# Kernel tuning notes

Measured on AMD Instinct MI355X. Metric: run time of the kernel, lower is better.

The kernel has to match this reference:

```python
import jax, jax.numpy as jnp
from jax import lax
import numpy as np

K = 3          # sampling grid size (kernel_size)
WS = 4         # scope kernel size (weight_shape)
DILATION = 1


def setup_inputs() -> dict:
    key = jax.random.key(0)
    k1, k2, k3, k4 = jax.random.split(key, 4)
    x = jax.random.normal(k1, (4, 128, 56, 56), jnp.float32)
    # offset conv is zero-initialized in the original; use small values so offsets are realistic
    offset_w = jax.random.normal(k2, (2 * K * K, 128, K, K), jnp.float32) * 0.01
    offset_b = jax.random.normal(k3, (2 * K * K,), jnp.float32) * 0.01
    weight = jax.random.normal(k4, (128, WS, WS), jnp.float32) * 0.1  # depthwise scope kernel
    return {"x": x, "offset_w": offset_w, "offset_b": offset_b, "weight": weight}


def reference(x, offset_w, offset_b, weight):
    B, C, H, W = x.shape
    K2 = K * K
    # offset conv: 3x3, stride 1, pad 1 (same geometry as main conv)
    off = lax.conv_general_dilated(
        x, offset_w, window_strides=(1, 1), padding=[(1, 1), (1, 1)],
        dimension_numbers=("NCHW", "OIHW", "NCHW"))
    off = off + offset_b[None, :, None, None]
    off = off * DILATION                     # offset_clip is None
    off = off.reshape(B, K2, 2, H, W)
    dy, dx = off[:, :, 0], off[:, :, 1]      # [B,K2,H,W]

    # base coordinates of the KxK sampling grid centered inside the WSxWS scope kernel
    base = jnp.arange(K, dtype=x.dtype) - (K - 1) / 2 + (WS - 1) / 2   # [K]
    by = jnp.repeat(base, K)                 # k = i*K + j -> row i
    bx = jnp.tile(base, K)                   # k = i*K + j -> col j
    yc = dy + by[None, :, None, None]        # [B,K2,H,W] sampling coords in kernel space
    xc = dx + bx[None, :, None, None]

    # bilinear sampling of the scope kernel (zero outside scope)
    wflat = weight.reshape(C, WS * WS)
    y0 = jnp.floor(yc)
    x0 = jnp.floor(xc)
    samp = jnp.zeros((C, B, K2, H, W), x.dtype)
    for oy, ox in ((0, 0), (0, 1), (1, 0), (1, 1)):
        yi = y0 + oy
        xi = x0 + ox
        coef = (1.0 - jnp.abs(yc - yi)) * (1.0 - jnp.abs(xc - xi))
        valid = (yi >= 0) & (yi < WS) & (xi >= 0) & (xi < WS)
        idx = (jnp.clip(yi, 0, WS - 1) * WS + jnp.clip(xi, 0, WS - 1)).astype(jnp.int32)
        vals = jnp.take(wflat, idx, axis=1)  # [C,B,K2,H,W] irregular gather
        samp = samp + (coef * valid)[None] * vals
    samp = jnp.moveaxis(samp, 0, 1)          # [B,C,K2,H,W]

    # depthwise conv with per-pixel sampled kernels (stride 1, pad 1, dilation 1)
    xp = jnp.pad(x, ((0, 0), (0, 0), (1, 1), (1, 1)))
    pats = jnp.stack([xp[:, :, i:i + H, j:j + W] for i in range(K) for j in range(K)], axis=2)
    return jnp.sum(samp * pats, axis=2)      # [B,C,H,W]
```

## Files before the change

### kernel.cpp

```cpp
#include <hip/hip_runtime.h>

#define CC 128
#define HH 56
#define WW 56
#define NK2 9
#define NO 18
#define WSZ 4
#define W64 64
#define NCG 16
#define SCG 8
#define CPG 16

#define WSA_FLOATS (224L * NCG * NO * W64)
#define WSC_ENTRIES (4L * NK2 * HH * W64)

__global__ __launch_bounds__(256, 4) void conv_partial(
    const float* __restrict__ x,
    const float* __restrict__ offset_w,
    float* __restrict__ wsA)
{
    const int blk = blockIdx.x;
    const int cg  = blk & 15;
    const int bh4 = blk >> 4;
    const int b   = bh4 / 14;
    const int h4  = bh4 - b * 14;
    const int h0  = h4 * 4;
    const int t   = threadIdx.x;
    const int lane = t & 63;
    const int wv  = __builtin_amdgcn_readfirstlane(t >> 6);

    __shared__ float s_red[4][2][NO][W64];

    float acc[4][NO];
    #pragma unroll
    for (int r = 0; r < 4; ++r)
        #pragma unroll
        for (int o = 0; o < NO; ++o) acc[r][o] = 0.f;

    if (lane < WW) {
        #pragma unroll
        for (int ci = 0; ci < 2; ++ci) {
            const int c = cg * 8 + wv * 2 + ci;
            const float* xc = x + ((long)b * CC + c) * HH * WW;
            float xr[6][3];
            #pragma unroll
            for (int r6 = 0; r6 < 6; ++r6) {
                const int hy = h0 + r6 - 1;
                float v0 = 0.f, v1 = 0.f, v2 = 0.f;
                if (hy >= 0 && hy < HH) {
                    const float* row = xc + hy * WW;
                    v1 = row[lane];
                    v0 = (lane > 0)      ? row[lane - 1] : 0.f;
                    v2 = (lane < WW - 1) ? row[lane + 1] : 0.f;
                }
                xr[r6][0] = v0; xr[r6][1] = v1; xr[r6][2] = v2;
            }
            const float* wc = offset_w + c * 9;
            #pragma unroll
            for (int o = 0; o < NO; ++o) {
                const float* wo = wc + o * (CC * 9);
                float w9[9];
                #pragma unroll
                for (int j = 0; j < 9; ++j) w9[j] = wo[j];
                #pragma unroll
                for (int ky = 0; ky < 3; ++ky)
                    #pragma unroll
                    for (int kx = 0; kx < 3; ++kx) {
                        const float wf = w9[ky * 3 + kx];
                        #pragma unroll
                        for (int r = 0; r < 4; ++r)
                            acc[r][o] += wf * xr[r + ky][kx];
                    }
            }
        }
    }

    const float* sr = (const float*)s_red;
    #pragma unroll
    for (int round = 0; round < 2; ++round) {
        #pragma unroll
        for (int r2 = 0; r2 < 2; ++r2)
            #pragma unroll
            for (int o = 0; o < NO; ++o)
                s_red[wv][r2][o][lane] = acc[round * 2 + r2][o];
        __syncthreads();
        for (int s = t; s < 2 * NO * W64; s += 256) {
            const float v = sr[s] + sr[2304 + s] + sr[2 * 2304 + s] + sr[3 * 2304 + s];
            const int r2  = s / (NO * W64);
            const int rem = s - r2 * (NO * W64);
            const int bh  = b * HH + h0 + round * 2 + r2;
            wsA[((long)bh * NCG + cg) * (NO * W64) + rem] = v;
        }
        __syncthreads();
    }
}

__global__ __launch_bounds__(64) void coef_kernel(
    const float* __restrict__ wsA,
    const float* __restrict__ offset_b,
    float4* __restrict__ wsC,
    unsigned* __restrict__ wsI)
{
    const int blk = blockIdx.x;
    const int k2  = blk % NK2;
    const int bh  = blk / NK2;
    const int b   = bh / HH;
    const int h   = bh - b * HH;
    const int w   = threadIdx.x;

    const float* base = wsA + (long)bh * (NCG * NO * W64);
    float dy = offset_b[2 * k2];
    float dx = offset_b[2 * k2 + 1];
    #pragma unroll
    for (int g = 0; g < NCG; ++g) {
        dy += base[g * (NO * W64) + (2 * k2) * W64 + w];
        dx += base[g * (NO * W64) + (2 * k2 + 1) * W64 + w];
    }

    const float yc = dy + 0.5f + (float)(k2 / 3);
    const float xc = dx + 0.5f + (float)(k2 % 3);
    const float y0 = floorf(yc), x0f = floorf(xc);
    const float fy = yc - y0, fx = xc - x0f;
    const int yi = (int)y0, xi = (int)x0f;
    float cf[4]; int id[4];
    #pragma unroll
    for (int q = 0; q < 4; ++q) {
        const int oy = q >> 1, ox = q & 1;
        const int yy = yi + oy, xx = xi + ox;
        float c2 = (oy ? fy : 1.f - fy) * (ox ? fx : 1.f - fx);
        const bool valid = (yy >= 0) && (yy < WSZ) && (xx >= 0) && (xx < WSZ);
        cf[q] = valid ? c2 : 0.f;
        const int yyc = yy < 0 ? 0 : (yy > 3 ? 3 : yy);
        const int xxc = xx < 0 ? 0 : (xx > 3 ? 3 : xx);
        id[q] = yyc * 4 + xxc;
    }
    const long oidx = ((long)(b * NK2 + k2) * HH + h) * W64 + w;
    wsC[oidx] = make_float4(cf[0], cf[1], cf[2], cf[3]);
    wsI[oidx] = (unsigned)(id[0] | (id[1] << 4) | (id[2] << 8) | (id[3] << 12));
}

__global__ __launch_bounds__(256) void sample_kernel(
    const float* __restrict__ x,
    const float* __restrict__ weight,
    const float4* __restrict__ wsC,
    const unsigned* __restrict__ wsI,
    float* __restrict__ out)
{
    const int blk = blockIdx.x;
    const int bh  = blk >> 3;
    const int cg  = blk & 7;
    const int b   = bh / HH;
    const int h   = bh - b * HH;
    const int t   = threadIdx.x;
    const int lane = t & 63;
    const int wv  = __builtin_amdgcn_readfirstlane(t >> 6);

    __shared__ float s_wT[16][20];
    if (t < 256) {
        const int j = t >> 4, cl = t & 15;
        s_wT[j][cl] = weight[(cg * CPG + cl) * 16 + j];
    }
    __syncthreads();

    if (lane >= WW) return;
    const int w = lane;
    const int cl0 = wv * 4;

    float4 cf[NK2]; unsigned pk[NK2];
    const long cidx0 = ((long)b * NK2 * HH + h) * W64 + w;
    #pragma unroll
    for (int k2 = 0; k2 < NK2; ++k2) {
        cf[k2] = wsC[cidx0 + (long)k2 * HH * W64];
        pk[k2] = wsI[cidx0 + (long)k2 * HH * W64];
    }

    float xv[4][9];
    #pragma unroll
    for (int u = 0; u < 4; ++u) {
        const int c = cg * CPG + cl0 + u;
        const float* xc = x + ((long)b * CC + c) * HH * WW;
        #pragma unroll
        for (int ky = 0; ky < 3; ++ky) {
            const int hy = h + ky - 1;
            #pragma unroll
            for (int kx = 0; kx < 3; ++kx) {
                const int wx = w + kx - 1;
                float v = 0.f;
                if (hy >= 0 && hy < HH && wx >= 0 && wx < WW)
                    v = xc[hy * WW + wx];
                xv[u][ky * 3 + kx] = v;
            }
        }
    }

    float res[4] = {0.f, 0.f, 0.f, 0.f};
    #pragma unroll
    for (int k2 = 0; k2 < NK2; ++k2) {
        const unsigned p = pk[k2];
        const float4 W0 = *(const float4*)&s_wT[p & 15][cl0];
        const float4 W1 = *(const float4*)&s_wT[(p >> 4) & 15][cl0];
        const float4 W2 = *(const float4*)&s_wT[(p >> 8) & 15][cl0];
        const float4 W3 = *(const float4*)&s_wT[(p >> 12) & 15][cl0];
        const float4 c4 = cf[k2];
        res[0] += (c4.x * W0.x + c4.y * W1.x + c4.z * W2.x + c4.w * W3.x) * xv[0][k2];
        res[1] += (c4.x * W0.y + c4.y * W1.y + c4.z * W2.y + c4.w * W3.y) * xv[1][k2];
        res[2] += (c4.x * W0.z + c4.y * W1.z + c4.z * W2.z + c4.w * W3.z) * xv[2][k2];
        res[3] += (c4.x * W0.w + c4.y * W1.w + c4.z * W2.w + c4.w * W3.w) * xv[3][k2];
    }

    #pragma unroll
    for (int u = 0; u < 4; ++u) {
        const int c = cg * CPG + cl0 + u;
        out[(((long)b * CC + c) * HH + h) * WW + w] = res[u];
    }
}

extern "C" void kernel_launch(void* const* d_in, const int* in_sizes, int n_in,
                              void* d_out, int out_size, void* d_ws, size_t ws_size,
                              hipStream_t stream) {
    const float* x        = (const float*)d_in[0];
    const float* offset_w = (const float*)d_in[1];
    const float* offset_b = (const float*)d_in[2];
    const float* weight   = (const float*)d_in[3];
    float* out = (float*)d_out;

    char* p = (char*)d_ws;
    float*    wsA = (float*)p;                          p += WSA_FLOATS * 4;
    float4*   wsC = (float4*)p;                         p += WSC_ENTRIES * 16;
    unsigned* wsI = (unsigned*)p;

    conv_partial <<<4 * 14 * NCG, 256, 0, stream>>>(x, offset_w, wsA);
    coef_kernel  <<<224 * NK2, 64, 0, stream>>>(wsA, offset_b, wsC, wsI);
    sample_kernel<<<224 * SCG, 256, 0, stream>>>(x, weight, wsC, wsI, out);
}
```

Before: 95.41 us.

## Stage input rows in LDS and split offset channels across twice the waves

The offset-conv partial kernel now runs 512 threads per block and splits the 18 output offset channels into two halves of 9, with each pair of waves sharing the same 2 input channels. Input rows, including halo and zero padding, are loaded once into shared memory instead of through per-lane global loads with boundary branches. This halves the per-thread accumulator count, which lowers register pressure and doubles the wave parallelism on this stage. In exchange it adds an extra barrier and shared-memory staging, and the larger blocks may limit occupancy.

```diff
diff --git a/kernel.cpp b/kernel.cpp
--- a/kernel.cpp
+++ b/kernel.cpp
@@ -14,7 +14,7 @@
 #define WSA_FLOATS (224L * NCG * NO * W64)
 #define WSC_ENTRIES (4L * NK2 * HH * W64)
 
-__global__ __launch_bounds__(256, 4) void conv_partial(
+__global__ __launch_bounds__(512, 4) void conv_partial(
     const float* __restrict__ x,
     const float* __restrict__ offset_w,
     float* __restrict__ wsA)
@@ -29,49 +29,62 @@
     const int lane = t & 63;
     const int wv  = __builtin_amdgcn_readfirstlane(t >> 6);
 
+    __shared__ float s_x[8][6][68];
     __shared__ float s_red[4][2][NO][W64];
 
-    float acc[4][NO];
+    const int c0 = cg * 8;
+
+    for (int i = t; i < 8 * 6 * 68; i += 512) {
+        const int cl  = i / 408;
+        const int rem = i - cl * 408;
+        const int r6  = rem / 68;
+        const int col = rem - r6 * 68;
+        const int wx  = col - 1;
+        const int hy  = h0 + r6 - 1;
+        float v = 0.f;
+        if (wx >= 0 && wx < WW && hy >= 0 && hy < HH)
+            v = x[(((long)b * CC + c0 + cl) * HH + hy) * WW + wx];
+        s_x[cl][r6][col] = v;
+    }
+    __syncthreads();
+
+    const int pair = wv >> 1;
+    const int half = wv & 1;
+
+    float acc[4][9];
     #pragma unroll
     for (int r = 0; r < 4; ++r)
         #pragma unroll
-        for (int o = 0; o < NO; ++o) acc[r][o] = 0.f;
-
-    if (lane < WW) {
-        #pragma unroll
-        for (int ci = 0; ci < 2; ++ci) {
-            const int c = cg * 8 + wv * 2 + ci;
-            const float* xc = x + ((long)b * CC + c) * HH * WW;
-            float xr[6][3];
-            #pragma unroll
-            for (int r6 = 0; r6 < 6; ++r6) {
-                const int hy = h0 + r6 - 1;
-                float v0 = 0.f, v1 = 0.f, v2 = 0.f;
-                if (hy >= 0 && hy < HH) {
-                    const float* row = xc + hy * WW;
-                    v1 = row[lane];
-                    v0 = (lane > 0)      ? row[lane - 1] : 0.f;
-                    v2 = (lane < WW - 1) ? row[lane + 1] : 0.f;
+        for (int oo = 0; oo < 9; ++oo) acc[r][oo] = 0.f;
+
+    #pragma unroll
+    for (int cl2 = 0; cl2 < 2; ++cl2) {
+        const int cl = pair * 2 + cl2;
+        const int c  = c0 + cl;
+
+        float xr[6][3];
+        #pragma unroll
+        for (int r6 = 0; r6 < 6; ++r6)
+            #pragma unroll
+            for (int k = 0; k < 3; ++k)
+                xr[r6][k] = s_x[cl][r6][lane + k];
+
+        const float* wc = offset_w + ((long)half * 9 * CC + c) * 9;
+        #pragma unroll
+        for (int oo = 0; oo < 9; ++oo) {
+            const float* wo = wc + oo * (CC * 9);
+            float w9[9];
+            #pragma unroll
+            for (int j = 0; j < 9; ++j) w9[j] = wo[j];
+            #pragma unroll
+            for (int ky = 0; ky < 3; ++ky)
+                #pragma unroll
+                for (int kx = 0; kx < 3; ++kx) {
+                    const float wf = w9[ky * 3 + kx];
+                    #pragma unroll
+                    for (int r = 0; r < 4; ++r)
+                        acc[r][oo] += wf * xr[r + ky][kx];
                 }
-                xr[r6][0] = v0; xr[r6][1] = v1; xr[r6][2] = v2;
-            }
-            const float* wc = offset_w + c * 9;
-            #pragma unroll
-            for (int o = 0; o < NO; ++o) {
-                const float* wo = wc + o * (CC * 9);
-                float w9[9];
-                #pragma unroll
-                for (int j = 0; j < 9; ++j) w9[j] = wo[j];
-                #pragma unroll
-                for (int ky = 0; ky < 3; ++ky)
-                    #pragma unroll
-                    for (int kx = 0; kx < 3; ++kx) {
-                        const float wf = w9[ky * 3 + kx];
-                        #pragma unroll
-                        for (int r = 0; r < 4; ++r)
-                            acc[r][o] += wf * xr[r + ky][kx];
-                    }
-            }
         }
     }
 
@@ -81,10 +94,10 @@
         #pragma unroll
         for (int r2 = 0; r2 < 2; ++r2)
             #pragma unroll
-            for (int o = 0; o < NO; ++o)
-                s_red[wv][r2][o][lane] = acc[round * 2 + r2][o];
+            for (int oo = 0; oo < 9; ++oo)
+                s_red[pair][r2][half * 9 + oo][lane] = acc[round * 2 + r2][oo];
         __syncthreads();
-        for (int s = t; s < 2 * NO * W64; s += 256) {
+        for (int s = t; s < 2 * NO * W64; s += 512) {
             const float v = sr[s] + sr[2304 + s] + sr[2 * 2304 + s] + sr[3 * 2304 + s];
             const int r2  = s / (NO * W64);
             const int rem = s - r2 * (NO * W64);
@@ -229,7 +242,7 @@
     float4*   wsC = (float4*)p;                         p += WSC_ENTRIES * 16;
     unsigned* wsI = (unsigned*)p;
 
-    conv_partial <<<4 * 14 * NCG, 256, 0, stream>>>(x, offset_w, wsA);
+    conv_partial <<<4 * 14 * NCG, 512, 0, stream>>>(x, offset_w, wsA);
     coef_kernel  <<<224 * NK2, 64, 0, stream>>>(wsA, offset_b, wsC, wsI);
     sample_kernel<<<224 * SCG, 256, 0, stream>>>(x, weight, wsC, wsI, out);
 }
```

Result: slower. 99.91 us (+4.7%).

## Compute offset conv with bf16 MFMA and fuse coefficient computation

Applied to the files above, without the earlier changes.

Replaces the scalar FP32 offset convolution and its separate partial-sum reduction and coefficient kernels with one kernel per output row. That kernel stages x in LDS as bf16 and runs the 3x3 conv as an implicit GEMM on 16x16x32 bf16 MFMA instructions. Bilinear coefficients are then computed directly from the LDS results. A small prep kernel repacks offset_w into MFMA A-fragment layout each call. This removes the global workspace round-trip and one launch, but lowers offset precision to bf16, which can shift floor() boundaries in the sampling coordinates.

```diff
diff --git a/kernel.cpp b/kernel.cpp
--- a/kernel.cpp
+++ b/kernel.cpp
@@ -7,136 +7,123 @@
 #define NO 18
 #define WSZ 4
 #define W64 64
-#define NCG 16
 #define SCG 8
 #define CPG 16
 
-#define WSA_FLOATS (224L * NCG * NO * W64)
+typedef __attribute__((ext_vector_type(8))) short short8;
+typedef __attribute__((ext_vector_type(4))) float f32x4;
+
+#define WSW_SHORTS  (9L * 2 * 4 * 64 * 8)
 #define WSC_ENTRIES (4L * NK2 * HH * W64)
 
-__global__ __launch_bounds__(256, 4) void conv_partial(
+__device__ __forceinline__ unsigned short f2bf(float f) {
+    unsigned u = __builtin_bit_cast(unsigned, f);
+    u = u + 0x7fffu + ((u >> 16) & 1u);
+    return (unsigned short)(u >> 16);
+}
+
+__global__ __launch_bounds__(256) void prep_afrag(
+    const float* __restrict__ offset_w,
+    unsigned short* __restrict__ wsW)
+{
+    const int e = blockIdx.x * 256 + threadIdx.x;
+    if (e >= (int)WSW_SHORTS) return;
+    const int j    = e & 7;
+    const int lane = (e >> 3) & 63;
+    const int kt   = (e >> 9) & 3;
+    const int mt   = (e >> 11) & 1;
+    const int k9   = e >> 12;
+    const int o = mt * 16 + (lane & 15);
+    const int c = kt * 32 + (lane >> 4) * 8 + j;
+    float v = 0.f;
+    if (o < NO) v = offset_w[(o * CC + c) * 9 + k9];
+    wsW[e] = f2bf(v);
+}
+
+__global__ __launch_bounds__(512) void conv_mfma(
     const float* __restrict__ x,
-    const float* __restrict__ offset_w,
-    float* __restrict__ wsA)
-{
-    const int blk = blockIdx.x;
-    const int cg  = blk & 15;
-    const int bh4 = blk >> 4;
-    const int b   = bh4 / 14;
-    const int h4  = bh4 - b * 14;
-    const int h0  = h4 * 4;
-    const int t   = threadIdx.x;
-    const int lane = t & 63;
-    const int wv  = __builtin_amdgcn_readfirstlane(t >> 6);
-
-    __shared__ float s_red[4][2][NO][W64];
-
-    float acc[4][NO];
-    #pragma unroll
-    for (int r = 0; r < 4; ++r)
-        #pragma unroll
-        for (int o = 0; o < NO; ++o) acc[r][o] = 0.f;
-
-    if (lane < WW) {
-        #pragma unroll
-        for (int ci = 0; ci < 2; ++ci) {
-            const int c = cg * 8 + wv * 2 + ci;
-            const float* xc = x + ((long)b * CC + c) * HH * WW;
-            float xr[6][3];
-            #pragma unroll
-            for (int r6 = 0; r6 < 6; ++r6) {
-                const int hy = h0 + r6 - 1;
-                float v0 = 0.f, v1 = 0.f, v2 = 0.f;
-                if (hy >= 0 && hy < HH) {
-                    const float* row = xc + hy * WW;
-                    v1 = row[lane];
-                    v0 = (lane > 0)      ? row[lane - 1] : 0.f;
-                    v2 = (lane < WW - 1) ? row[lane + 1] : 0.f;
-                }
-                xr[r6][0] = v0; xr[r6][1] = v1; xr[r6][2] = v2;
-            }
-            const float* wc = offset_w + c * 9;
-            #pragma unroll
-            for (int o = 0; o < NO; ++o) {
-                const float* wo = wc + o * (CC * 9);
-                float w9[9];
-                #pragma unroll
-                for (int j = 0; j < 9; ++j) w9[j] = wo[j];
-                #pragma unroll
-                for (int ky = 0; ky < 3; ++ky)
-                    #pragma unroll
-                    for (int kx = 0; kx < 3; ++kx) {
-                        const float wf = w9[ky * 3 + kx];
-                        #pragma unroll
-                        for (int r = 0; r < 4; ++r)
-                            acc[r][o] += wf * xr[r + ky][kx];
-                    }
-            }
-        }
-    }
-
-    const float* sr = (const float*)s_red;
-    #pragma unroll
-    for (int round = 0; round < 2; ++round) {
-        #pragma unroll
-        for (int r2 = 0; r2 < 2; ++r2)
-            #pragma unroll
-            for (int o = 0; o < NO; ++o)
-                s_red[wv][r2][o][lane] = acc[round * 2 + r2][o];
-        __syncthreads();
-        for (int s = t; s < 2 * NO * W64; s += 256) {
-            const float v = sr[s] + sr[2304 + s] + sr[2 * 2304 + s] + sr[3 * 2304 + s];
-            const int r2  = s / (NO * W64);
-            const int rem = s - r2 * (NO * W64);
-            const int bh  = b * HH + h0 + round * 2 + r2;
-            wsA[((long)bh * NCG + cg) * (NO * W64) + rem] = v;
-        }
-        __syncthreads();
-    }
-}
-
-__global__ __launch_bounds__(64) void coef_kernel(
-    const float* __restrict__ wsA,
+    const unsigned short* __restrict__ wsW,
     const float* __restrict__ offset_b,
     float4* __restrict__ wsC,
     unsigned* __restrict__ wsI)
 {
     const int blk = blockIdx.x;
-    const int k2  = blk % NK2;
-    const int bh  = blk / NK2;
-    const int b   = bh / HH;
-    const int h   = bh - b * HH;
-    const int w   = threadIdx.x;
-
-    const float* base = wsA + (long)bh * (NCG * NO * W64);
-    float dy = offset_b[2 * k2];
-    float dx = offset_b[2 * k2 + 1];
-    #pragma unroll
-    for (int g = 0; g < NCG; ++g) {
-        dy += base[g * (NO * W64) + (2 * k2) * W64 + w];
-        dx += base[g * (NO * W64) + (2 * k2 + 1) * W64 + w];
-    }
-
-    const float yc = dy + 0.5f + (float)(k2 / 3);
-    const float xc = dx + 0.5f + (float)(k2 % 3);
-    const float y0 = floorf(yc), x0f = floorf(xc);
-    const float fy = yc - y0, fx = xc - x0f;
-    const int yi = (int)y0, xi = (int)x0f;
-    float cf[4]; int id[4];
-    #pragma unroll
-    for (int q = 0; q < 4; ++q) {
-        const int oy = q >> 1, ox = q & 1;
-        const int yy = yi + oy, xx = xi + ox;
-        float c2 = (oy ? fy : 1.f - fy) * (ox ? fx : 1.f - fx);
-        const bool valid = (yy >= 0) && (yy < WSZ) && (xx >= 0) && (xx < WSZ);
-        cf[q] = valid ? c2 : 0.f;
-        const int yyc = yy < 0 ? 0 : (yy > 3 ? 3 : yy);
-        const int xxc = xx < 0 ? 0 : (xx > 3 ? 3 : xx);
-        id[q] = yyc * 4 + xxc;
-    }
-    const long oidx = ((long)(b * NK2 + k2) * HH + h) * W64 + w;
-    wsC[oidx] = make_float4(cf[0], cf[1], cf[2], cf[3]);
-    wsI[oidx] = (unsigned)(id[0] | (id[1] << 4) | (id[2] << 8) | (id[3] << 12));
+    const int b = blk / HH;
+    const int h = blk - b * HH;
+    const int t = threadIdx.x;
+    const int lane = t & 63;
+    const int wv = t >> 6;
+
+    __shared__ unsigned short s_xb[3][58][136];
+    __shared__ float s_off[NO][W64];
+
+    for (int i = t; i < 3 * CC * 58; i += 512) {
+        const int r   = i / (CC * 58);
+        const int rem = i - r * (CC * 58);
+        const int c   = rem / 58;
+        const int col = rem - c * 58;
+        const int hy = h + r - 1;
+        const int w  = col - 1;
+        float v = 0.f;
+        if (hy >= 0 && hy < HH && w >= 0 && w < WW)
+            v = x[(((long)b * CC + c) * HH + hy) * WW + w];
+        s_xb[r][col][c] = f2bf(v);
+    }
+    __syncthreads();
+
+    const int nt  = wv & 3;
+    const int mt  = wv >> 2;
+    const int q   = lane >> 4;
+    const int n15 = lane & 15;
+
+    f32x4 acc = {0.f, 0.f, 0.f, 0.f};
+    #pragma unroll
+    for (int k9 = 0; k9 < 9; ++k9) {
+        const int ky = k9 / 3, kx = k9 - ky * 3;
+        int col = nt * 16 + n15 + kx;
+        col = col > 57 ? 57 : col;
+        const unsigned short* bbase = &s_xb[ky][col][q * 8];
+        const unsigned short* abase = wsW + ((long)(k9 * 2 + mt) * 4 * 64 + lane) * 8;
+        #pragma unroll
+        for (int kt = 0; kt < 4; ++kt) {
+            short8 a  = *(const short8*)(abase + kt * 512);
+            short8 bf = *(const short8*)(bbase + kt * 32);
+            acc = __builtin_amdgcn_mfma_f32_16x16x32_bf16(a, bf, acc, 0, 0, 0);
+        }
+    }
+    #pragma unroll
+    for (int reg = 0; reg < 4; ++reg) {
+        const int o = mt * 16 + q * 4 + reg;
+        if (o < NO) s_off[o][nt * 16 + n15] = acc[reg];
+    }
+    __syncthreads();
+
+    for (int i = t; i < NK2 * 64; i += 512) {
+        const int k2 = i >> 6;
+        const int px = i & 63;
+        const float dy = s_off[2 * k2][px]     + offset_b[2 * k2];
+        const float dx = s_off[2 * k2 + 1][px] + offset_b[2 * k2 + 1];
+        const float yc = dy + 0.5f + (float)(k2 / 3);
+        const float xc = dx + 0.5f + (float)(k2 % 3);
+        const float y0 = floorf(yc), x0f = floorf(xc);
+        const float fy = yc - y0, fx = xc - x0f;
+        const int yi = (int)y0, xi = (int)x0f;
+        float cf[4]; int id[4];
+        #pragma unroll
+        for (int qq = 0; qq < 4; ++qq) {
+            const int oy = qq >> 1, ox = qq & 1;
+            const int yy = yi + oy, xx = xi + ox;
+            float c2 = (oy ? fy : 1.f - fy) * (ox ? fx : 1.f - fx);
+            const bool valid = (yy >= 0) && (yy < WSZ) && (xx >= 0) && (xx < WSZ);
+            cf[qq] = valid ? c2 : 0.f;
+            const int yyc = yy < 0 ? 0 : (yy > 3 ? 3 : yy);
+            const int xxc = xx < 0 ? 0 : (xx > 3 ? 3 : xx);
+            id[qq] = yyc * 4 + xxc;
+        }
+        const long oidx = ((long)(b * NK2 + k2) * HH + h) * W64 + px;
+        wsC[oidx] = make_float4(cf[0], cf[1], cf[2], cf[3]);
+        wsI[oidx] = (unsigned)(id[0] | (id[1] << 4) | (id[2] << 8) | (id[3] << 12));
+    }
 }
 
 __global__ __launch_bounds__(256) void sample_kernel(
@@ -225,11 +212,11 @@
     float* out = (float*)d_out;
 
     char* p = (char*)d_ws;
-    float*    wsA = (float*)p;                          p += WSA_FLOATS * 4;
-    float4*   wsC = (float4*)p;                         p += WSC_ENTRIES * 16;
-    unsigned* wsI = (unsigned*)p;
-
-    conv_partial <<<4 * 14 * NCG, 256, 0, stream>>>(x, offset_w, wsA);
-    coef_kernel  <<<224 * NK2, 64, 0, stream>>>(wsA, offset_b, wsC, wsI);
+    unsigned short* wsW = (unsigned short*)p;           p += WSW_SHORTS * 2;
+    float4*         wsC = (float4*)p;                   p += WSC_ENTRIES * 16;
+    unsigned*       wsI = (unsigned*)p;
+
+    prep_afrag   <<<(int)(WSW_SHORTS / 256), 256, 0, stream>>>(offset_w, wsW);
+    conv_mfma    <<<4 * HH, 512, 0, stream>>>(x, wsW, offset_b, wsC, wsI);
     sample_kernel<<<224 * SCG, 256, 0, stream>>>(x, weight, wsC, wsI, out);
 }
```

Result: no change. 96.03 us (+0.6%).
